# Performance work log

Measured on AMD Instinct MI355X. Metric: run time of the kernel, lower is better.

## Reference

```python
import jax, jax.numpy as jnp
import numpy as np

VOCAB = 50265
D = 768
N_NEW = 200          # rows in new_embedding before zero-pad row
N_NODES = N_NEW - 1  # GAT operates on new_emb[1:-1]
N_EDGES = 1024
B, S = 8, 4096
LEAKY_SLOPE = 0.2


def setup_inputs() -> dict:
    key = jax.random.key(0)
    ks = jax.random.split(key, 7)
    x = jax.random.randint(ks[0], (B, S), 0, VOCAB + N_NEW, dtype=jnp.int32)
    orig_emb = jax.random.normal(ks[1], (VOCAB, D), dtype=jnp.float32) * 0.02
    new_emb = jax.random.normal(ks[2], (N_NEW + 1, D), dtype=jnp.float32) * 0.02
    new_emb = new_emb.at[0].set(0.0)  # prepended zero/pad row, as in __init__
    W = jax.random.normal(ks[3], (D, D), dtype=jnp.float32) * (1.0 / np.sqrt(D))
    a_src = jax.random.normal(ks[4], (D,), dtype=jnp.float32) * 0.1
    a_dst = jax.random.normal(ks[5], (D,), dtype=jnp.float32) * 0.1
    edge_index = jax.random.randint(ks[6], (2, N_EDGES), 0, N_NODES, dtype=jnp.int32)
    return {"x": x, "orig_emb": orig_emb, "new_emb": new_emb, "W": W,
            "a_src": a_src, "a_dst": a_dst, "edge_index": edge_index}


def _gat(feats, W, a_src, a_dst, edge_index):
    # Single-layer GAT over the label graph (edge list form, no dense NxN).
    h = feats @ W                                   # [N, D]
    src, dst = edge_index[0], edge_index[1]
    e = jax.nn.leaky_relu(h[src] @ a_src + h[dst] @ a_dst, LEAKY_SLOPE)  # [E]
    m = jax.ops.segment_max(e, dst, num_segments=N_NODES)               # stable softmax
    ex = jnp.exp(e - m[dst])
    denom = jax.ops.segment_sum(ex, dst, num_segments=N_NODES)
    alpha = ex / jnp.maximum(denom[dst], 1e-9)                          # [E]
    agg = jax.ops.segment_sum(alpha[:, None] * h[src], dst, num_segments=N_NODES)
    return jax.nn.elu(agg) + feats                  # residual, [N, D]


def reference(x, orig_emb, new_emb, W, a_src, a_dst, edge_index):
    # weight(): graph-encode new rows 1:-1, re-append last row, concat with vocab table
    node_feats = new_emb[1:-1]                      # [N_NODES, D]
    graph_feats = _gat(node_feats, W, a_src, a_dst, edge_index)
    table = jnp.concatenate([orig_emb, graph_feats, new_emb[-1:]], axis=0)  # [VOCAB+N_NEW, D]
    # F.embedding(x, table, padding_idx) forward is a plain gather
    return table[x]                                 # [B, S, D]
```

## Files before the change

kernel.cpp:

```cpp
#include <hip/hip_runtime.h>
#include <math.h>

#define VOCAB   50265
#define D       768
#define N_NEW   200
#define N_NODES 199
#define N_EDGES 1024
#define LEAKY   0.2f

typedef float f4 __attribute__((ext_vector_type(4)));

#define ROW_T 4
#define KC    8
#define KLEN  96
#define NROWT 50
#define NCH   (KC * 3)

__global__ __launch_bounds__(256) void gemm_partial_kernel(
    const float* __restrict__ new_emb, const float* __restrict__ W,
    const float* __restrict__ a_src, const float* __restrict__ a_dst,
    float* __restrict__ partial, float* __restrict__ svp, float* __restrict__ dvp)
{
    __shared__ float fts[ROW_T][KLEN];
    __shared__ float rS[ROW_T][4], rD[ROW_T][4];
    const int tid  = threadIdx.x;
    const int rowt = blockIdx.x;
    const int colt = blockIdx.y;
    const int kc   = blockIdx.z;
    const int row0 = rowt * ROW_T;
    const int col  = colt * 256 + tid;
    const int k0   = kc * KLEN;
    const int lane = tid & 63, wid = tid >> 6;

    for (int i = tid; i < ROW_T * KLEN; i += 256) {
        int r  = i / KLEN;
        int kk = i - r * KLEN;
        int row = row0 + r;
        fts[r][kk] = (row < N_NODES) ? new_emb[(size_t)(1 + row) * D + k0 + kk] : 0.f;
    }
    __syncthreads();

    float acc[ROW_T] = {0.f, 0.f, 0.f, 0.f};
    #pragma unroll 4
    for (int kk = 0; kk < KLEN; ++kk) {
        float w = W[(size_t)(k0 + kk) * D + col];
        #pragma unroll
        for (int r = 0; r < ROW_T; ++r)
            acc[r] = fmaf(fts[r][kk], w, acc[r]);
    }

    const size_t base = ((size_t)kc * N_NODES) * D + col;
    #pragma unroll
    for (int r = 0; r < ROW_T; ++r)
        if (row0 + r < N_NODES) partial[base + (size_t)(row0 + r) * D] = acc[r];

    const float as = a_src[col];
    const float ad = a_dst[col];
    #pragma unroll
    for (int r = 0; r < ROW_T; ++r) {
        float ps = acc[r] * as;
        float pd = acc[r] * ad;
        #pragma unroll
        for (int off = 32; off; off >>= 1) {
            ps += __shfl_down(ps, off, 64);
            pd += __shfl_down(pd, off, 64);
        }
        if (lane == 0) { rS[r][wid] = ps; rD[r][wid] = pd; }
    }
    __syncthreads();
    if (tid < ROW_T) {
        const int row = row0 + tid;
        if (row < N_NODES) {
            const int slot = row * NCH + kc * 3 + colt;
            svp[slot] = rS[tid][0] + rS[tid][1] + rS[tid][2] + rS[tid][3];
            dvp[slot] = rD[tid][0] + rD[tid][1] + rD[tid][2] + rD[tid][3];
        }
    }
}

__global__ __launch_bounds__(256) void softagg_kernel(
    const int* __restrict__ edge_index, const float* __restrict__ svp,
    const float* __restrict__ dvp, const float* __restrict__ partial,
    const float* __restrict__ new_emb, float* __restrict__ gfeats)
{
    __shared__ float sv_l[N_NODES], dv_l[N_NODES];
    __shared__ float e[N_EDGES];
    __shared__ short ssrc[N_EDGES];
    __shared__ short ml[N_EDGES];
    __shared__ int   wsum[4];
    __shared__ int   s_total;
    const int n   = blockIdx.x;
    const int tid = threadIdx.x;
    const int lane = tid & 63, wid = tid >> 6;

    for (int i = tid; i < N_NODES; i += 256) {
        float s = 0.f, d = 0.f;
        #pragma unroll
        for (int q = 0; q < NCH; ++q) {
            s += svp[i * NCH + q];
            d += dvp[i * NCH + q];
        }
        sv_l[i] = s;
        dv_l[i] = d;
    }
    __syncthreads();

    const int4 se = ((const int4*)edge_index)[tid];
    const int4 de = ((const int4*)(edge_index + N_EDGES))[tid];
    const int srcs[4] = { se.x, se.y, se.z, se.w };
    const int dsts[4] = { de.x, de.y, de.z, de.w };

    int mycnt = 0;
    #pragma unroll
    for (int j = 0; j < 4; ++j) {
        const int k = 4 * tid + j;
        float ev = sv_l[srcs[j]] + dv_l[dsts[j]];
        e[k] = ev > 0.f ? ev : LEAKY * ev;
        ssrc[k] = (short)srcs[j];
        if (dsts[j] == n) ++mycnt;
    }

    int pre = mycnt;
    #pragma unroll
    for (int off = 1; off < 64; off <<= 1) {
        int v = __shfl_up(pre, off, 64);
        if (lane >= off) pre += v;
    }
    if (lane == 63) wsum[wid] = pre;
    __syncthreads();
    int woff = 0;
    for (int w = 0; w < wid; ++w) woff += wsum[w];
    int base = woff + pre - mycnt;
    #pragma unroll
    for (int j = 0; j < 4; ++j) {
        if (dsts[j] == n) ml[base++] = (short)(4 * tid + j);
    }
    if (tid == 255) s_total = woff + pre;
    __syncthreads();

    const int c = s_total;

    float mx = -INFINITY;
    for (int p = 0; p < c; ++p) mx = fmaxf(mx, e[ml[p]]);
    float dn = 0.f;
    for (int p = 0; p < c; ++p) dn += expf(e[ml[p]] - mx);
    const float inv = 1.f / fmaxf(dn, 1e-9f);

    const size_t kcstride = (size_t)N_NODES * D;
    float a0 = 0.f, a1 = 0.f, a2 = 0.f;
    for (int p = 0; p < c; ++p) {
        const int k = ml[p];
        const float a = expf(e[k] - mx) * inv;
        const float* pb = partial + (size_t)ssrc[k] * D;
        float h0 = 0.f, h1 = 0.f, h2 = 0.f;
        #pragma unroll
        for (int q = 0; q < KC; ++q) {
            h0 += pb[q * kcstride + tid];
            h1 += pb[q * kcstride + tid + 256];
            h2 += pb[q * kcstride + tid + 512];
        }
        a0 = fmaf(a, h0, a0);
        a1 = fmaf(a, h1, a1);
        a2 = fmaf(a, h2, a2);
    }
    const float* f = new_emb + (size_t)(1 + n) * D;
    float e0 = a0 > 0.f ? a0 : expf(a0) - 1.f;
    float e1 = a1 > 0.f ? a1 : expf(a1) - 1.f;
    float e2 = a2 > 0.f ? a2 : expf(a2) - 1.f;
    gfeats[(size_t)n * D + tid]       = e0 + f[tid];
    gfeats[(size_t)n * D + tid + 256] = e1 + f[tid + 256];
    gfeats[(size_t)n * D + tid + 512] = e2 + f[tid + 512];
}

__global__ __launch_bounds__(256) void gather_kernel(
    const int* __restrict__ x, const float* __restrict__ orig_emb,
    const float* __restrict__ gfeats, const float* __restrict__ new_emb,
    float* __restrict__ out, int ntok)
{
    const int token = blockIdx.x * 4 + (threadIdx.x >> 6);
    if (token >= ntok) return;
    const int lane = threadIdx.x & 63;
    const int idx = x[token];

    const f4* src;
    if (idx < VOCAB)
        src = (const f4*)(orig_emb + (size_t)idx * D);
    else if (idx < VOCAB + N_NODES)
        src = (const f4*)(gfeats + (size_t)(idx - VOCAB) * D);
    else
        src = (const f4*)(new_emb + (size_t)N_NEW * D);

    f4* dst = (f4*)(out + (size_t)token * D);
    f4 v0 = src[lane];
    f4 v1 = src[lane + 64];
    f4 v2 = src[lane + 128];
    __builtin_nontemporal_store(v0, &dst[lane]);
    __builtin_nontemporal_store(v1, &dst[lane + 64]);
    __builtin_nontemporal_store(v2, &dst[lane + 128]);
}

extern "C" void kernel_launch(void* const* d_in, const int* in_sizes, int n_in,
                              void* d_out, int out_size, void* d_ws, size_t ws_size,
                              hipStream_t stream) {
    const int*   x        = (const int*)  d_in[0];
    const float* orig_emb = (const float*)d_in[1];
    const float* new_emb  = (const float*)d_in[2];
    const float* W        = (const float*)d_in[3];
    const float* a_src    = (const float*)d_in[4];
    const float* a_dst    = (const float*)d_in[5];
    const int*   edge_idx = (const int*)  d_in[6];
    float* out = (float*)d_out;

    float* ws      = (float*)d_ws;
    float* partial = ws;
    float* svp     = partial + (size_t)KC * N_NODES * D;
    float* dvp     = svp + N_NODES * NCH;
    float* gfeats  = dvp + N_NODES * NCH;

    const int ntok = in_sizes[0];

    gemm_partial_kernel<<<dim3(NROWT, 3, KC), 256, 0, stream>>>(
        new_emb, W, a_src, a_dst, partial, svp, dvp);
    softagg_kernel<<<N_NODES, 256, 0, stream>>>(
        edge_idx, svp, dvp, partial, new_emb, gfeats);
    gather_kernel<<<(ntok + 3) / 4, 256, 0, stream>>>(
        x, orig_emb, gfeats, new_emb, out, ntok);
}
```

Measured before the change: 59.76 us.

## Overlap vocab gather with GAT GEMM and defer graph-row tokens to fixup

Merges the GEMM-partial blocks and the bulk embedding-gather blocks into one hybrid launch, so the large token gather no longer waits behind the GAT computation. Tokens that index graph-encoded rows are appended to a global list with an atomic, and a small fixup kernel copies them after softagg produces the graph features. The aim is to hide the GAT GEMM and softmax latency behind the memory-bound gather. The cost is an extra memset launch and atomics, and the GEMM blocks now share the machine with gather blocks.

```diff
diff --git a/kernel.cpp b/kernel.cpp
--- a/kernel.cpp
+++ b/kernel.cpp
@@ -15,67 +15,101 @@
 #define KLEN  96
 #define NROWT 50
 #define NCH   (KC * 3)
-
-__global__ __launch_bounds__(256) void gemm_partial_kernel(
+#define NB_GEMM (NROWT * 3 * KC)
+
+__global__ __launch_bounds__(256) void hybrid_kernel(
+    const int* __restrict__ x, const float* __restrict__ orig_emb,
     const float* __restrict__ new_emb, const float* __restrict__ W,
     const float* __restrict__ a_src, const float* __restrict__ a_dst,
-    float* __restrict__ partial, float* __restrict__ svp, float* __restrict__ dvp)
+    float* __restrict__ partial, float* __restrict__ svp, float* __restrict__ dvp,
+    float* __restrict__ out, int* __restrict__ gcnt, int* __restrict__ glist,
+    int ntok)
 {
-    __shared__ float fts[ROW_T][KLEN];
-    __shared__ float rS[ROW_T][4], rD[ROW_T][4];
-    const int tid  = threadIdx.x;
-    const int rowt = blockIdx.x;
-    const int colt = blockIdx.y;
-    const int kc   = blockIdx.z;
-    const int row0 = rowt * ROW_T;
-    const int col  = colt * 256 + tid;
-    const int k0   = kc * KLEN;
-    const int lane = tid & 63, wid = tid >> 6;
-
-    for (int i = tid; i < ROW_T * KLEN; i += 256) {
-        int r  = i / KLEN;
-        int kk = i - r * KLEN;
-        int row = row0 + r;
-        fts[r][kk] = (row < N_NODES) ? new_emb[(size_t)(1 + row) * D + k0 + kk] : 0.f;
-    }
-    __syncthreads();
-
-    float acc[ROW_T] = {0.f, 0.f, 0.f, 0.f};
-    #pragma unroll 4
-    for (int kk = 0; kk < KLEN; ++kk) {
-        float w = W[(size_t)(k0 + kk) * D + col];
+    const int tid = threadIdx.x;
+    const int bid = blockIdx.x;
+
+    if (bid < NB_GEMM) {
+        __shared__ float fts[ROW_T][KLEN];
+        __shared__ float rS[ROW_T][4], rD[ROW_T][4];
+        const int rowt = bid % NROWT;
+        const int colt = (bid / NROWT) % 3;
+        const int kc   = bid / (NROWT * 3);
+        const int row0 = rowt * ROW_T;
+        const int col  = colt * 256 + tid;
+        const int k0   = kc * KLEN;
+        const int lane = tid & 63, wid = tid >> 6;
+
+        for (int i = tid; i < ROW_T * KLEN; i += 256) {
+            int r  = i / KLEN;
+            int kk = i - r * KLEN;
+            int row = row0 + r;
+            fts[r][kk] = (row < N_NODES) ? new_emb[(size_t)(1 + row) * D + k0 + kk] : 0.f;
+        }
+        __syncthreads();
+
+        float acc[ROW_T] = {0.f, 0.f, 0.f, 0.f};
+        #pragma unroll 4
+        for (int kk = 0; kk < KLEN; ++kk) {
+            float w = W[(size_t)(k0 + kk) * D + col];
+            #pragma unroll
+            for (int r = 0; r < ROW_T; ++r)
+                acc[r] = fmaf(fts[r][kk], w, acc[r]);
+        }
+
+        const size_t base = ((size_t)kc * N_NODES) * D + col;
         #pragma unroll
         for (int r = 0; r < ROW_T; ++r)
-            acc[r] = fmaf(fts[r][kk], w, acc[r]);
-    }
-
-    const size_t base = ((size_t)kc * N_NODES) * D + col;
-    #pragma unroll
-    for (int r = 0; r < ROW_T; ++r)
-        if (row0 + r < N_NODES) partial[base + (size_t)(row0 + r) * D] = acc[r];
-
-    const float as = a_src[col];
-    const float ad = a_dst[col];
-    #pragma unroll
-    for (int r = 0; r < ROW_T; ++r) {
-        float ps = acc[r] * as;
-        float pd = acc[r] * ad;
-        #pragma unroll
-        for (int off = 32; off; off >>= 1) {
-            ps += __shfl_down(ps, off, 64);
-            pd += __shfl_down(pd, off, 64);
-        }
-        if (lane == 0) { rS[r][wid] = ps; rD[r][wid] = pd; }
-    }
-    __syncthreads();
-    if (tid < ROW_T) {
-        const int row = row0 + tid;
-        if (row < N_NODES) {
-            const int slot = row * NCH + kc * 3 + colt;
-            svp[slot] = rS[tid][0] + rS[tid][1] + rS[tid][2] + rS[tid][3];
-            dvp[slot] = rD[tid][0] + rD[tid][1] + rD[tid][2] + rD[tid][3];
-        }
-    }
+            if (row0 + r < N_NODES) partial[base + (size_t)(row0 + r) * D] = acc[r];
+
+        const float as = a_src[col];
+        const float ad = a_dst[col];
+        #pragma unroll
+        for (int r = 0; r < ROW_T; ++r) {
+            float ps = acc[r] * as;
+            float pd = acc[r] * ad;
+            #pragma unroll
+            for (int off = 32; off; off >>= 1) {
+                ps += __shfl_down(ps, off, 64);
+                pd += __shfl_down(pd, off, 64);
+            }
+            if (lane == 0) { rS[r][wid] = ps; rD[r][wid] = pd; }
+        }
+        __syncthreads();
+        if (tid < ROW_T) {
+            const int row = row0 + tid;
+            if (row < N_NODES) {
+                const int slot = row * NCH + kc * 3 + colt;
+                svp[slot] = rS[tid][0] + rS[tid][1] + rS[tid][2] + rS[tid][3];
+                dvp[slot] = rD[tid][0] + rD[tid][1] + rD[tid][2] + rD[tid][3];
+            }
+        }
+        return;
+    }
+
+    const int token = (bid - NB_GEMM) * 4 + (tid >> 6);
+    if (token >= ntok) return;
+    const int lane = tid & 63;
+    const int idx = x[token];
+
+    if (idx >= VOCAB && idx < VOCAB + N_NODES) {
+        if (lane == 0) {
+            int pos = atomicAdd(gcnt, 1);
+            glist[pos] = token;
+        }
+        return;
+    }
+
+    const f4* src = (idx < VOCAB)
+        ? (const f4*)(orig_emb + (size_t)idx * D)
+        : (const f4*)(new_emb + (size_t)N_NEW * D);
+
+    f4* dst = (f4*)(out + (size_t)token * D);
+    f4 v0 = src[lane];
+    f4 v1 = src[lane + 64];
+    f4 v2 = src[lane + 128];
+    __builtin_nontemporal_store(v0, &dst[lane]);
+    __builtin_nontemporal_store(v1, &dst[lane + 64]);
+    __builtin_nontemporal_store(v2, &dst[lane + 128]);
 }
 
 __global__ __launch_bounds__(256) void softagg_kernel(
@@ -172,31 +206,28 @@
     gfeats[(size_t)n * D + tid + 512] = e2 + f[tid + 512];
 }
 
-__global__ __launch_bounds__(256) void gather_kernel(
-    const int* __restrict__ x, const float* __restrict__ orig_emb,
-    const float* __restrict__ gfeats, const float* __restrict__ new_emb,
-    float* __restrict__ out, int ntok)
+#define FIX_BLOCKS 64
+__global__ __launch_bounds__(256) void fixup_kernel(
+    const int* __restrict__ x, const float* __restrict__ gfeats,
+    const int* __restrict__ gcnt, const int* __restrict__ glist,
+    float* __restrict__ out)
 {
-    const int token = blockIdx.x * 4 + (threadIdx.x >> 6);
-    if (token >= ntok) return;
     const int lane = threadIdx.x & 63;
-    const int idx = x[token];
-
-    const f4* src;
-    if (idx < VOCAB)
-        src = (const f4*)(orig_emb + (size_t)idx * D);
-    else if (idx < VOCAB + N_NODES)
-        src = (const f4*)(gfeats + (size_t)(idx - VOCAB) * D);
-    else
-        src = (const f4*)(new_emb + (size_t)N_NEW * D);
-
-    f4* dst = (f4*)(out + (size_t)token * D);
-    f4 v0 = src[lane];
-    f4 v1 = src[lane + 64];
-    f4 v2 = src[lane + 128];
-    __builtin_nontemporal_store(v0, &dst[lane]);
-    __builtin_nontemporal_store(v1, &dst[lane + 64]);
-    __builtin_nontemporal_store(v2, &dst[lane + 128]);
+    const int wid  = threadIdx.x >> 6;
+    const int cnt  = *gcnt;
+
+    for (int i = blockIdx.x * 4 + wid; i < cnt; i += FIX_BLOCKS * 4) {
+        const int token = glist[i];
+        const int n = x[token] - VOCAB;
+        const f4* src = (const f4*)(gfeats + (size_t)n * D);
+        f4* dst = (f4*)(out + (size_t)token * D);
+        f4 v0 = src[lane];
+        f4 v1 = src[lane + 64];
+        f4 v2 = src[lane + 128];
+        __builtin_nontemporal_store(v0, &dst[lane]);
+        __builtin_nontemporal_store(v1, &dst[lane + 64]);
+        __builtin_nontemporal_store(v2, &dst[lane + 128]);
+    }
 }
 
 extern "C" void kernel_launch(void* const* d_in, const int* in_sizes, int n_in,
@@ -211,18 +242,22 @@
     const int*   edge_idx = (const int*)  d_in[6];
     float* out = (float*)d_out;
 
-    float* ws      = (float*)d_ws;
-    float* partial = ws;
+    int*   gcnt    = (int*)d_ws;
+    float* partial = (float*)((char*)d_ws + 256);
     float* svp     = partial + (size_t)KC * N_NODES * D;
     float* dvp     = svp + N_NODES * NCH;
     float* gfeats  = dvp + N_NODES * NCH;
+    int*   glist   = (int*)(gfeats + (size_t)N_NODES * D);
 
     const int ntok = in_sizes[0];
-
-    gemm_partial_kernel<<<dim3(NROWT, 3, KC), 256, 0, stream>>>(
-        new_emb, W, a_src, a_dst, partial, svp, dvp);
+    const int nblocks = NB_GEMM + (ntok + 3) / 4;
+
+    hipMemsetAsync(gcnt, 0, 16, stream);
+    hybrid_kernel<<<nblocks, 256, 0, stream>>>(
+        x, orig_emb, new_emb, W, a_src, a_dst,
+        partial, svp, dvp, out, gcnt, glist, ntok);
     softagg_kernel<<<N_NODES, 256, 0, stream>>>(
         edge_idx, svp, dvp, partial, new_emb, gfeats);
-    gather_kernel<<<(ntok + 3) / 4, 256, 0, stream>>>(
-        x, orig_emb, gfeats, new_emb, out, ntok);
-}
+    fixup_kernel<<<FIX_BLOCKS, 256, 0, stream>>>(
+        x, gfeats, gcnt, glist, out);
+}
```

Result: faster. 56.88 us (-4.8%).
